# Performance work log

Measured on AMD Instinct MI355X. Metric: run time of the kernel, lower is better.

## Reference

```python
import jax, jax.numpy as jnp
import numpy as np

B, S, D, H = 2, 4096, 512, 8
DK = D // H  # 64

def setup_inputs() -> dict:
    key = jax.random.key(0)
    k1, k2, k3, k4 = jax.random.split(key, 4)
    return {
        "queries": jax.random.normal(k1, (B, S, D), dtype=jnp.float32),
        "keys": jax.random.normal(k2, (B, S, D), dtype=jnp.float32),
        "values": jax.random.normal(k3, (B, S, D), dtype=jnp.float32),
        "W_o": jax.random.normal(k4, (D, D), dtype=jnp.float32) * (1.0 / np.sqrt(D)),
        "b_o": jnp.zeros((D,), dtype=jnp.float32),
    }

def reference(queries, keys, values, W_o, b_o):
    b_s, nq, _ = queries.shape
    nk = keys.shape[1]
    # split heads: (b, s, h, dk) -> (b, h, s, dk)
    q = queries.reshape(b_s, nq, H, DK).transpose(0, 2, 1, 3)
    k = keys.reshape(b_s, nk, H, DK).transpose(0, 2, 1, 3)
    v = values.reshape(b_s, nk, H, DK).transpose(0, 2, 1, 3)
    # full (nq, nk) attention matrix, scaled by sqrt(d_k)
    att = jnp.einsum("bhqd,bhkd->bhqk", q, k) / np.sqrt(DK).astype(np.float32)
    att = jax.nn.softmax(att, axis=-1)  # dropout is identity at inference
    out = jnp.einsum("bhqk,bhkd->bhqd", att, v)
    out = out.transpose(0, 2, 1, 3).reshape(b_s, nq, H * DK)
    return out @ W_o + b_o
```

## Files before the change

### kernel.cpp

```cpp
#include <hip/hip_runtime.h>
#include <hip/hip_bf16.h>

#define Bn 2
#define Sn 4096
#define Dn 512
#define Hn 8

typedef _Float16 f16x8 __attribute__((ext_vector_type(8)));
typedef __fp16 fp16x2 __attribute__((ext_vector_type(2)));
typedef float f32x16 __attribute__((ext_vector_type(16)));
typedef unsigned uint2v __attribute__((ext_vector_type(2)));

static __device__ __forceinline__ unsigned pkh(float a, float b) {
    union { fp16x2 h; unsigned u; } r;
    r.h = __builtin_amdgcn_cvt_pkrtz(a, b);
    return r.u;
}

static __device__ __forceinline__ f16x8 xchg2(unsigned g0x, unsigned g0y,
                                              unsigned g1x, unsigned g1y, int hi) {
    union { unsigned u[4]; f16x8 v; } f;
#if __has_builtin(__builtin_amdgcn_permlane32_swap)
    uint2v rx = __builtin_amdgcn_permlane32_swap(g0x, g1x, false, false);
    uint2v ry = __builtin_amdgcn_permlane32_swap(g0y, g1y, false, false);
    f.u[0] = rx.x; f.u[1] = ry.x; f.u[2] = rx.y; f.u[3] = ry.y;
#else
    int sx = hi ? (int)g0x : (int)g1x;
    int sy = hi ? (int)g0y : (int)g1y;
    int rx = __shfl_xor(sx, 32);
    int ry = __shfl_xor(sy, 32);
    unsigned ox = hi ? g1x : g0x;
    unsigned oy = hi ? g1y : g0y;
    f.u[0] = hi ? (unsigned)rx : ox;
    f.u[1] = hi ? (unsigned)ry : oy;
    f.u[2] = hi ? ox : (unsigned)rx;
    f.u[3] = hi ? oy : (unsigned)ry;
#endif
    return f.v;
}

__global__ __launch_bounds__(256) void prep_kernel(
    const float* __restrict__ K, const float* __restrict__ V, const float* __restrict__ W,
    unsigned short* __restrict__ Kb, unsigned short* __restrict__ Vb,
    unsigned short* __restrict__ Wb) {
    const int vb = blockIdx.x;
    const int tid = threadIdx.x;
    if (vb < 1024) {
        const int kt = vb & 63, bh = vb >> 6;
        const int b = bh >> 3, h = bh & 7;
        unsigned short* dst = Kb + ((size_t)bh * 64 + kt) * 4096;
#pragma unroll
        for (int i = 0; i < 2; ++i) {
            int c = tid + i * 256;
            int f = c >> 6, ln = c & 63;
            int ktile = f >> 2, ks = f & 3;
            int row = ktile * 32 + (ln & 31);
            int dk = ks * 16 + (ln >> 5) * 8;
            const float* src = K + ((size_t)(b * Sn + kt * 64 + row)) * Dn + h * 64 + dk;
            float4 a0 = *(const float4*)src;
            float4 a1 = *(const float4*)(src + 4);
            uint4 o;
            o.x = pkh(a0.x, a0.y); o.y = pkh(a0.z, a0.w);
            o.z = pkh(a1.x, a1.y); o.w = pkh(a1.z, a1.w);
            *(uint4*)(dst + c * 8) = o;
        }
    } else if (vb < 2048) {
        const int u = vb - 1024;
        const int kt = u & 63, bh = u >> 6;
        const int b = bh >> 3, h = bh & 7;
        unsigned short* dst = Vb + ((size_t)bh * 64 + kt) * 4096;
#pragma unroll
        for (int i = 0; i < 2; ++i) {
            int c = tid + i * 256;
            int f = c >> 6, ln = c & 63;
            int dt = f >> 2, ks = f & 3;
            int dk = dt * 32 + (ln & 31);
            int key0 = ks * 16 + (ln >> 5) * 8;
            const float* src = V + ((size_t)(b * Sn + kt * 64 + key0)) * Dn + h * 64 + dk;
            uint4 o;
            o.x = pkh(src[0 * Dn], src[1 * Dn]);
            o.y = pkh(src[2 * Dn], src[3 * Dn]);
            o.z = pkh(src[4 * Dn], src[5 * Dn]);
            o.w = pkh(src[6 * Dn], src[7 * Dn]);
            *(uint4*)(dst + c * 8) = o;
        }
    } else {
        int c = (vb - 2048) * 256 + tid;
        int ln = c & 63, f = c >> 6;
        int ntile = f >> 5, ks = f & 31;
        int n = ntile * 32 + (ln & 31);
        int k0 = ks * 16 + (ln >> 5) * 8;
        uint4 o;
        o.x = pkh(W[(size_t)(k0 + 0) * Dn + n], W[(size_t)(k0 + 1) * Dn + n]);
        o.y = pkh(W[(size_t)(k0 + 2) * Dn + n], W[(size_t)(k0 + 3) * Dn + n]);
        o.z = pkh(W[(size_t)(k0 + 4) * Dn + n], W[(size_t)(k0 + 5) * Dn + n]);
        o.w = pkh(W[(size_t)(k0 + 6) * Dn + n], W[(size_t)(k0 + 7) * Dn + n]);
        *(uint4*)(Wb + c * 8) = o;
    }
}

__global__ __launch_bounds__(512, 4) void attn_kernel(
    const float* __restrict__ Q,
    const unsigned short* __restrict__ Kb,
    const unsigned short* __restrict__ Vb,
    unsigned short* __restrict__ ObA) {
    __shared__ __align__(16) unsigned short KV[32768];

    const int qt = blockIdx.x;
    const int bh = blockIdx.y;
    const int b = bh >> 3, h = bh & 7;
    const int tid = threadIdx.x;
    const int wg = tid >> 6;
    const int half = wg >> 2;
    const int w4 = wg & 3;
    const int lane = tid & 63;
    const int q = lane & 31;
    const int hi = lane >> 5;
    const int q0 = qt * 128 + w4 * 32;
    const int th = tid & 255;
    const float cexp = 0.18033688f;

    f16x8 qf[4];
    {
        const float* qp = Q + ((size_t)(b * Sn + q0 + q)) * Dn + h * 64 + hi * 8;
#pragma unroll
        for (int ks = 0; ks < 4; ++ks) {
            float4 a0 = *(const float4*)(qp + ks * 16);
            float4 a1 = *(const float4*)(qp + ks * 16 + 4);
            union { unsigned u[4]; f16x8 v; } f;
            f.u[0] = pkh(a0.x * cexp, a0.y * cexp);
            f.u[1] = pkh(a0.z * cexp, a0.w * cexp);
            f.u[2] = pkh(a1.x * cexp, a1.y * cexp);
            f.u[3] = pkh(a1.z * cexp, a1.w * cexp);
            qf[ks] = f.v;
        }
    }

    f32x16 zf;
#pragma unroll
    for (int r = 0; r < 16; ++r) zf[r] = 0.f;
    f32x16 oacc[2];
    oacc[0] = zf; oacc[1] = zf;
    float l_ = 0.f;

    const size_t tbase = ((size_t)bh * 64 + half * 32) * 4096;
    const unsigned short* kg = Kb + tbase;
    const unsigned short* vg = Vb + tbase;

    {
        uint4 a = *(const uint4*)(kg + th * 16);
        uint4 c = *(const uint4*)(kg + th * 16 + 8);
        uint4 d = *(const uint4*)(vg + th * 16);
        uint4 e2 = *(const uint4*)(vg + th * 16 + 8);
        unsigned short* Kb0 = KV + half * 4096;
        unsigned short* Vb0 = KV + 8192 + half * 4096;
        *(uint4*)&Kb0[th * 16] = a;
        *(uint4*)&Kb0[th * 16 + 8] = c;
        *(uint4*)&Vb0[th * 16] = d;
        *(uint4*)&Vb0[th * 16 + 8] = e2;
    }
    uint4 gk0 = *(const uint4*)(kg + 4096 + th * 16);
    uint4 gk1 = *(const uint4*)(kg + 4096 + th * 16 + 8);
    uint4 gv0 = *(const uint4*)(vg + 4096 + th * 16);
    uint4 gv1 = *(const uint4*)(vg + 4096 + th * 16 + 8);

    for (int it = 0; it < 32; ++it) {
        __syncthreads();
        const unsigned short* Kbuf = KV + (it & 1) * 16384 + half * 4096;
        const unsigned short* Vbuf = KV + (it & 1) * 16384 + 8192 + half * 4096;

#pragma unroll
        for (int t = 0; t < 2; ++t) {
            f16x8 ka = *(const f16x8*)&Kbuf[(t * 4 + 0) * 512 + lane * 8];
            f32x16 sa = __builtin_amdgcn_mfma_f32_32x32x16_f16(ka, qf[0], zf, 0, 0, 0);
#pragma unroll
            for (int ks = 1; ks < 4; ++ks) {
                ka = *(const f16x8*)&Kbuf[(t * 4 + ks) * 512 + lane * 8];
                sa = __builtin_amdgcn_mfma_f32_32x32x16_f16(ka, qf[ks], sa, 0, 0, 0);
            }
            float e[16];
            float s0 = 0.f, s1 = 0.f;
#pragma unroll
            for (int r = 0; r < 16; r += 2) {
                e[r] = __builtin_amdgcn_exp2f(sa[r]);
                e[r + 1] = __builtin_amdgcn_exp2f(sa[r + 1]);
                s0 += e[r]; s1 += e[r + 1];
            }
            l_ += s0 + s1;
#pragma unroll
            for (int s2 = 0; s2 < 2; ++s2) {
                unsigned g0x = pkh(e[8 * s2 + 0], e[8 * s2 + 1]);
                unsigned g0y = pkh(e[8 * s2 + 2], e[8 * s2 + 3]);
                unsigned g1x = pkh(e[8 * s2 + 4], e[8 * s2 + 5]);
                unsigned g1y = pkh(e[8 * s2 + 6], e[8 * s2 + 7]);
                f16x8 pb = xchg2(g0x, g0y, g1x, g1y, hi);
                const int kp = t * 2 + s2;
                f16x8 va0 = *(const f16x8*)&Vbuf[(0 * 4 + kp) * 512 + lane * 8];
                f16x8 va1 = *(const f16x8*)&Vbuf[(1 * 4 + kp) * 512 + lane * 8];
                oacc[0] = __builtin_amdgcn_mfma_f32_32x32x16_f16(va0, pb, oacc[0], 0, 0, 0);
                oacc[1] = __builtin_amdgcn_mfma_f32_32x32x16_f16(va1, pb, oacc[1], 0, 0, 0);
            }
        }

        if (it < 31) {
            unsigned short* nK = KV + ((it + 1) & 1) * 16384 + half * 4096;
            unsigned short* nV = KV + ((it + 1) & 1) * 16384 + 8192 + half * 4096;
            *(uint4*)&nK[th * 16] = gk0;
            *(uint4*)&nK[th * 16 + 8] = gk1;
            *(uint4*)&nV[th * 16] = gv0;
            *(uint4*)&nV[th * 16 + 8] = gv1;
            if (it < 30) {
                const unsigned short* ks_ = kg + (size_t)(it + 2) * 4096;
                const unsigned short* vs_ = vg + (size_t)(it + 2) * 4096;
                gk0 = *(const uint4*)(ks_ + th * 16);
                gk1 = *(const uint4*)(ks_ + th * 16 + 8);
                gv0 = *(const uint4*)(vs_ + th * 16);
                gv1 = *(const uint4*)(vs_ + th * 16 + 8);
            }
        }
    }

    __syncthreads();
    float* rp = (float*)KV + w4 * 2048;
    float* Ls = (float*)KV + 8192 + w4 * 64;
    if (half) {
#pragma unroll
        for (int g = 0; g < 8; ++g) {
            float4 v;
            v.x = oacc[g >> 2][(g & 3) * 4 + 0];
            v.y = oacc[g >> 2][(g & 3) * 4 + 1];
            v.z = oacc[g >> 2][(g & 3) * 4 + 2];
            v.w = oacc[g >> 2][(g & 3) * 4 + 3];
            *(float4*)&rp[g * 256 + lane * 4] = v;
        }
        Ls[lane] = l_;
    }
    __syncthreads();
    if (!half) {
#pragma unroll
        for (int g = 0; g < 8; ++g) {
            float4 v = *(const float4*)&rp[g * 256 + lane * 4];
            oacc[g >> 2][(g & 3) * 4 + 0] += v.x;
            oacc[g >> 2][(g & 3) * 4 + 1] += v.y;
            oacc[g >> 2][(g & 3) * 4 + 2] += v.z;
            oacc[g >> 2][(g & 3) * 4 + 3] += v.w;
        }
        l_ += Ls[lane];
        l_ += __shfl_xor(l_, 32);
        const float li = 1.f / l_;
        const int gm = b * 128 + qt * 4 + w4;
#pragma unroll
        for (int ksg = 0; ksg < 4; ++ksg) {
            const int dt = ksg >> 1, k2 = ksg & 1;
            unsigned g0x = pkh(oacc[dt][8 * k2 + 0] * li, oacc[dt][8 * k2 + 1] * li);
            unsigned g0y = pkh(oacc[dt][8 * k2 + 2] * li, oacc[dt][8 * k2 + 3] * li);
            unsigned g1x = pkh(oacc[dt][8 * k2 + 4] * li, oacc[dt][8 * k2 + 5] * li);
            unsigned g1y = pkh(oacc[dt][8 * k2 + 6] * li, oacc[dt][8 * k2 + 7] * li);
            f16x8 frag = xchg2(g0x, g0y, g1x, g1y, hi);
            union { f16x8 v; uint4 u; } fu; fu.v = frag;
            *(uint4*)&ObA[((size_t)(gm * 32 + h * 4 + ksg) * 64 + lane) * 8] = fu.u;
        }
    }
}

__global__ __launch_bounds__(256) void proj_kernel(
    const unsigned short* __restrict__ ObA,
    const unsigned short* __restrict__ Wb,
    const float* __restrict__ bias,
    float* __restrict__ out) {
    __shared__ __align__(16) unsigned short Ash[8192];
    __shared__ __align__(16) unsigned short Wsh[4096];

    const int mt = blockIdx.x;
    const int nt = blockIdx.y;
    const int tid = threadIdx.x;
    const int w = tid >> 6;
    const int lane = tid & 63;
    const int q = lane & 31;
    const int hi = lane >> 5;

    f32x16 acc[2];
#pragma unroll
    for (int t = 0; t < 2; ++t)
#pragma unroll
        for (int r = 0; r < 16; ++r) acc[t][r] = 0.f;

    for (int kt = 0; kt < 8; ++kt) {
        __syncthreads();
#pragma unroll
        for (int i = 0; i < 4; ++i) {
            int ci = (tid >> 6) + i * 4;
            int ml = ci >> 2, ksl = ci & 3;
            *(uint4*)&Ash[ci * 512 + lane * 8] =
                *(const uint4*)(ObA + (((size_t)(mt * 4 + ml) * 32 + kt * 4 + ksl) * 64 + lane) * 8);
        }
#pragma unroll
        for (int i = 0; i < 2; ++i) {
            int ci = (tid >> 6) + i * 4;
            int ntl = ci >> 2, ksl = ci & 3;
            *(uint4*)&Wsh[ci * 512 + lane * 8] =
                *(const uint4*)(Wb + (((size_t)(nt * 2 + ntl) * 32 + kt * 4 + ksl) * 64 + lane) * 8);
        }
        __syncthreads();

#pragma unroll
        for (int ks = 0; ks < 4; ++ks) {
            f16x8 a  = *(const f16x8*)&Ash[(w * 4 + ks) * 512 + lane * 8];
            f16x8 b0 = *(const f16x8*)&Wsh[(0 * 4 + ks) * 512 + lane * 8];
            f16x8 b1 = *(const f16x8*)&Wsh[(4 + ks) * 512 + lane * 8];
            acc[0] = __builtin_amdgcn_mfma_f32_32x32x16_f16(a, b0, acc[0], 0, 0, 0);
            acc[1] = __builtin_amdgcn_mfma_f32_32x32x16_f16(a, b1, acc[1], 0, 0, 0);
        }
    }

#pragma unroll
    for (int ntl = 0; ntl < 2; ++ntl) {
        int col = nt * 64 + ntl * 32 + q;
        float bv = bias[col];
#pragma unroll
        for (int reg = 0; reg < 16; ++reg) {
            int row = mt * 128 + w * 32 + (reg & 3) + 8 * (reg >> 2) + 4 * hi;
            out[(size_t)row * Dn + col] = acc[ntl][reg] + bv;
        }
    }
}

extern "C" void kernel_launch(void* const* d_in, const int* in_sizes, int n_in,
                              void* d_out, int out_size, void* d_ws, size_t ws_size,
                              hipStream_t stream) {
    const float* Q = (const float*)d_in[0];
    const float* K = (const float*)d_in[1];
    const float* V = (const float*)d_in[2];
    const float* W = (const float*)d_in[3];
    const float* bo = (const float*)d_in[4];
    float* out = (float*)d_out;

    char* ws = (char*)d_ws;
    unsigned short* Kb  = (unsigned short*)(ws);
    unsigned short* Vb  = (unsigned short*)(ws + 8388608);
    unsigned short* Wb  = (unsigned short*)(ws + 16777216);
    unsigned short* ObA = (unsigned short*)(ws + 17301504);

    prep_kernel<<<2176, 256, 0, stream>>>(K, V, W, Kb, Vb, Wb);
    attn_kernel<<<dim3(32, 16), 512, 0, stream>>>(Q, Kb, Vb, ObA);
    proj_kernel<<<dim3(64, 8), 256, 0, stream>>>(ObA, Wb, bo, out);
}
```

Measured before the change: 185.2 us.

## Stage K/V tiles with direct global-to-LDS loads and interleave QK MFMA chains

Replaces the register-staged K/V prefetch (global load to VGPRs, then LDS store) with global_load_lds DMA-style loads, issued per wave right after the barrier for the next buffer. It also computes both 32-key score tiles as two interleaved MFMA chains before the exp/PV phase, which adds independent MFMA work between dependent accumulates. The aim is to save VGPRs and LDS-store instructions and to hide MFMA latency. Loads now depend on the single barrier per iteration for correctness, with no explicit vmcnt wait before the LDS reads, so ordering relies on compiler or barrier semantics.

```diff
diff --git a/kernel.cpp b/kernel.cpp
--- a/kernel.cpp
+++ b/kernel.cpp
@@ -10,6 +10,17 @@
 typedef __fp16 fp16x2 __attribute__((ext_vector_type(2)));
 typedef float f32x16 __attribute__((ext_vector_type(16)));
 typedef unsigned uint2v __attribute__((ext_vector_type(2)));
+
+#if __has_builtin(__builtin_amdgcn_global_load_lds)
+#define HAS_GLL 1
+typedef const __attribute__((address_space(1))) unsigned int* gas1_t;
+typedef __attribute__((address_space(3))) unsigned int* las3_t;
+static __device__ __forceinline__ void ld_lds16(const void* g, void* l) {
+    __builtin_amdgcn_global_load_lds((gas1_t)g, (las3_t)l, 16, 0, 0);
+}
+#else
+#define HAS_GLL 0
+#endif
 
 static __device__ __forceinline__ unsigned pkh(float a, float b) {
     union { fp16x2 h; unsigned u; } r;
@@ -117,7 +128,6 @@
     const int q = lane & 31;
     const int hi = lane >> 5;
     const int q0 = qt * 128 + w4 * 32;
-    const int th = tid & 255;
     const float cexp = 0.18033688f;
 
     f16x8 qf[4];
@@ -144,79 +154,77 @@
     float l_ = 0.f;
 
     const size_t tbase = ((size_t)bh * 64 + half * 32) * 4096;
-    const unsigned short* kg = Kb + tbase;
-    const unsigned short* vg = Vb + tbase;
-
-    {
-        uint4 a = *(const uint4*)(kg + th * 16);
-        uint4 c = *(const uint4*)(kg + th * 16 + 8);
-        uint4 d = *(const uint4*)(vg + th * 16);
-        uint4 e2 = *(const uint4*)(vg + th * 16 + 8);
-        unsigned short* Kb0 = KV + half * 4096;
-        unsigned short* Vb0 = KV + 8192 + half * 4096;
-        *(uint4*)&Kb0[th * 16] = a;
-        *(uint4*)&Kb0[th * 16 + 8] = c;
-        *(uint4*)&Vb0[th * 16] = d;
-        *(uint4*)&Vb0[th * 16 + 8] = e2;
-    }
-    uint4 gk0 = *(const uint4*)(kg + 4096 + th * 16);
-    uint4 gk1 = *(const uint4*)(kg + 4096 + th * 16 + 8);
-    uint4 gv0 = *(const uint4*)(vg + 4096 + th * 16);
-    uint4 gv1 = *(const uint4*)(vg + 4096 + th * 16 + 8);
+    const unsigned short* kgw = Kb + tbase + w4 * 1024;
+    const unsigned short* vgw = Vb + tbase + w4 * 1024;
+    const int lK = half * 4096 + w4 * 1024;
+    const int lV = 8192 + half * 4096 + w4 * 1024;
+
+#if HAS_GLL
+#define STAGE(itx, bb) { \
+    const unsigned short* ksp = kgw + (size_t)(itx) * 4096 + lane * 8; \
+    const unsigned short* vsp = vgw + (size_t)(itx) * 4096 + lane * 8; \
+    unsigned short* lk = &KV[(bb) * 16384 + lK]; \
+    unsigned short* lv = &KV[(bb) * 16384 + lV]; \
+    ld_lds16(ksp, lk); ld_lds16(ksp + 512, lk + 512); \
+    ld_lds16(vsp, lv); ld_lds16(vsp + 512, lv + 512); }
+    STAGE(0, 0);
+#else
+    const int th = tid & 255;
+#define STAGE(itx, bb) { \
+    const unsigned short* ksp = kgw - (size_t)w4 * 1024 + (size_t)(itx) * 4096; \
+    const unsigned short* vsp = vgw - (size_t)w4 * 1024 + (size_t)(itx) * 4096; \
+    uint4 a0 = *(const uint4*)(ksp + th * 8); \
+    uint4 a1 = *(const uint4*)(ksp + 2048 + th * 8); \
+    uint4 a2 = *(const uint4*)(vsp + th * 8); \
+    uint4 a3 = *(const uint4*)(vsp + 2048 + th * 8); \
+    unsigned short* lk = &KV[(bb) * 16384 + half * 4096]; \
+    unsigned short* lv = &KV[(bb) * 16384 + 8192 + half * 4096]; \
+    *(uint4*)&lk[th * 8] = a0; *(uint4*)&lk[2048 + th * 8] = a1; \
+    *(uint4*)&lv[th * 8] = a2; *(uint4*)&lv[2048 + th * 8] = a3; }
+    STAGE(0, 0);
+#endif
 
     for (int it = 0; it < 32; ++it) {
         __syncthreads();
         const unsigned short* Kbuf = KV + (it & 1) * 16384 + half * 4096;
-        const unsigned short* Vbuf = KV + (it & 1) * 16384 + 8192 + half * 4096;
-
-#pragma unroll
-        for (int t = 0; t < 2; ++t) {
-            f16x8 ka = *(const f16x8*)&Kbuf[(t * 4 + 0) * 512 + lane * 8];
-            f32x16 sa = __builtin_amdgcn_mfma_f32_32x32x16_f16(ka, qf[0], zf, 0, 0, 0);
+        const unsigned short* Vbuf = Kbuf + 8192;
+        if (it < 31) STAGE(it + 1, (it + 1) & 1);
+
+        f32x16 sa0, sa1;
+        {
+            f16x8 ka = *(const f16x8*)&Kbuf[0 * 512 + lane * 8];
+            f16x8 kb = *(const f16x8*)&Kbuf[4 * 512 + lane * 8];
+            sa0 = __builtin_amdgcn_mfma_f32_32x32x16_f16(ka, qf[0], zf, 0, 0, 0);
+            sa1 = __builtin_amdgcn_mfma_f32_32x32x16_f16(kb, qf[0], zf, 0, 0, 0);
 #pragma unroll
             for (int ks = 1; ks < 4; ++ks) {
-                ka = *(const f16x8*)&Kbuf[(t * 4 + ks) * 512 + lane * 8];
-                sa = __builtin_amdgcn_mfma_f32_32x32x16_f16(ka, qf[ks], sa, 0, 0, 0);
+                ka = *(const f16x8*)&Kbuf[(0 + ks) * 512 + lane * 8];
+                kb = *(const f16x8*)&Kbuf[(4 + ks) * 512 + lane * 8];
+                sa0 = __builtin_amdgcn_mfma_f32_32x32x16_f16(ka, qf[ks], sa0, 0, 0, 0);
+                sa1 = __builtin_amdgcn_mfma_f32_32x32x16_f16(kb, qf[ks], sa1, 0, 0, 0);
             }
-            float e[16];
-            float s0 = 0.f, s1 = 0.f;
-#pragma unroll
-            for (int r = 0; r < 16; r += 2) {
-                e[r] = __builtin_amdgcn_exp2f(sa[r]);
-                e[r + 1] = __builtin_amdgcn_exp2f(sa[r + 1]);
-                s0 += e[r]; s1 += e[r + 1];
-            }
-            l_ += s0 + s1;
-#pragma unroll
-            for (int s2 = 0; s2 < 2; ++s2) {
-                unsigned g0x = pkh(e[8 * s2 + 0], e[8 * s2 + 1]);
-                unsigned g0y = pkh(e[8 * s2 + 2], e[8 * s2 + 3]);
-                unsigned g1x = pkh(e[8 * s2 + 4], e[8 * s2 + 5]);
-                unsigned g1y = pkh(e[8 * s2 + 6], e[8 * s2 + 7]);
-                f16x8 pb = xchg2(g0x, g0y, g1x, g1y, hi);
-                const int kp = t * 2 + s2;
-                f16x8 va0 = *(const f16x8*)&Vbuf[(0 * 4 + kp) * 512 + lane * 8];
-                f16x8 va1 = *(const f16x8*)&Vbuf[(1 * 4 + kp) * 512 + lane * 8];
-                oacc[0] = __builtin_amdgcn_mfma_f32_32x32x16_f16(va0, pb, oacc[0], 0, 0, 0);
-                oacc[1] = __builtin_amdgcn_mfma_f32_32x32x16_f16(va1, pb, oacc[1], 0, 0, 0);
-            }
-        }
-
-        if (it < 31) {
-            unsigned short* nK = KV + ((it + 1) & 1) * 16384 + half * 4096;
-            unsigned short* nV = KV + ((it + 1) & 1) * 16384 + 8192 + half * 4096;
-            *(uint4*)&nK[th * 16] = gk0;
-            *(uint4*)&nK[th * 16 + 8] = gk1;
-            *(uint4*)&nV[th * 16] = gv0;
-            *(uint4*)&nV[th * 16 + 8] = gv1;
-            if (it < 30) {
-                const unsigned short* ks_ = kg + (size_t)(it + 2) * 4096;
-                const unsigned short* vs_ = vg + (size_t)(it + 2) * 4096;
-                gk0 = *(const uint4*)(ks_ + th * 16);
-                gk1 = *(const uint4*)(ks_ + th * 16 + 8);
-                gv0 = *(const uint4*)(vs_ + th * 16);
-                gv1 = *(const uint4*)(vs_ + th * 16 + 8);
-            }
+        }
+        float e0[16], e1[16];
+        float s0 = 0.f, s1 = 0.f;
+#pragma unroll
+        for (int r = 0; r < 16; ++r) { e0[r] = __builtin_amdgcn_exp2f(sa0[r]); s0 += e0[r]; }
+#pragma unroll
+        for (int r = 0; r < 16; ++r) { e1[r] = __builtin_amdgcn_exp2f(sa1[r]); s1 += e1[r]; }
+        l_ += s0 + s1;
+
+#pragma unroll
+        for (int kp = 0; kp < 4; ++kp) {
+            const float* e = (kp < 2) ? e0 : e1;
+            const int s2 = kp & 1;
+            unsigned g0x = pkh(e[8 * s2 + 0], e[8 * s2 + 1]);
+            unsigned g0y = pkh(e[8 * s2 + 2], e[8 * s2 + 3]);
+            unsigned g1x = pkh(e[8 * s2 + 4], e[8 * s2 + 5]);
+            unsigned g1y = pkh(e[8 * s2 + 6], e[8 * s2 + 7]);
+            f16x8 pb = xchg2(g0x, g0y, g1x, g1y, hi);
+            f16x8 va0 = *(const f16x8*)&Vbuf[(0 + kp) * 512 + lane * 8];
+            f16x8 va1 = *(const f16x8*)&Vbuf[(4 + kp) * 512 + lane * 8];
+            oacc[0] = __builtin_amdgcn_mfma_f32_32x32x16_f16(va0, pb, oacc[0], 0, 0, 0);
+            oacc[1] = __builtin_amdgcn_mfma_f32_32x32x16_f16(va1, pb, oacc[1], 0, 0, 0);
         }
     }
 
```

Result: no change. 185.2 us (-0.0%).
